# Kernel optimization log

Hardware: AMD Instinct MI355X
Metric: run time of the kernel (lower is better)

Reference implementation:

```python
import jax, jax.numpy as jnp
import numpy as np

THRESH = 0.5
ALPHA = 1.0
LOG_CLAMP = -100.0  # torch BCELoss clamps log terms at -100


def setup_inputs() -> dict:
    key = jax.random.key(0)
    k1, k2 = jax.random.split(key)
    B, N, C = 2048, 2704, 5
    # predictions: confidences/boxes in (0,1) (post-sigmoid style)
    x = jax.random.uniform(k1, (B, N, C), dtype=jnp.float32, minval=1e-3, maxval=1.0 - 1e-3)
    # labels: conf in [0,1] (~half > 0.5 -> faces), boxes in [0,1]
    y = jax.random.uniform(k2, (B, N, C), dtype=jnp.float32)
    return {"x": x, "y": y}


def _clog(v):
    return jnp.maximum(jnp.log(v), LOG_CLAMP)


def reference(x, y):
    # x, y: [B, N, 5]; channel 0 = confidence, 1:5 = box
    mask = y[..., 0] > THRESH                      # [B, N] face cells
    face_num = jnp.sum(mask).astype(x.dtype)
    bg_num = mask.size - face_num
    scale = 1.0 + 1.0 / face_num

    # MSE over masked boxes, mean over (face_num * 4) elements
    sq = jnp.sum((x[..., 1:5] - y[..., 1:5]) ** 2, axis=-1)   # [B, N]
    diff_box = scale * jnp.sum(jnp.where(mask, sq, 0.0)) / (face_num * 4.0)

    # BCE(pred_conf, label_conf) over face cells, mean
    p = x[..., 0]
    t = y[..., 0]
    bce = -(t * _clog(p) + (1.0 - t) * _clog(1.0 - p))        # [B, N]
    diff_c = scale * jnp.sum(jnp.where(mask, bce, 0.0)) / face_num

    # BCE(pred_conf, 0) over background cells, mean
    bg_bce = -_clog(1.0 - p)                                  # [B, N]
    diff_bg = ALPHA * jnp.sum(jnp.where(mask, 0.0, bg_bce)) / bg_num

    return diff_box + diff_c + diff_bg
```

## Files before the change

kernel.cpp:

```cpp
#include <hip/hip_runtime.h>


#define BLOCK 256
#define CPT 4
#define FPT (CPT * 5)
#define F4PT (FPT / 4)
#define F4_PER_BLOCK (BLOCK * F4PT)
#define PAD_STRIDE (FPT + 1)
#define LDS_FLOATS (BLOCK * PAD_STRIDE)

#define LOG_CLAMP -100.0f
#define THRESH 0.5f

__device__ __forceinline__ float clogf(float v) {
    return fmaxf(logf(v), LOG_CLAMP);
}

__global__ __launch_bounds__(BLOCK) void mloss_reduce(
    const float* __restrict__ x, const float* __restrict__ y,
    float4* __restrict__ partials)
{
    __shared__ float lx[LDS_FLOATS];
    __shared__ float ly[LDS_FLOATS];

    const long long base_f4 = (long long)blockIdx.x * F4_PER_BLOCK;
    const float4* gx = (const float4*)x + base_f4;
    const float4* gy = (const float4*)y + base_f4;

    float4 vx[F4PT], vy[F4PT];
    #pragma unroll
    for (int k = 0; k < F4PT; ++k) {
        const int i4 = threadIdx.x + k * BLOCK;
        vx[k] = gx[i4];
        vy[k] = gy[i4];
    }
    #pragma unroll
    for (int k = 0; k < F4PT; ++k) {
        const int i4 = threadIdx.x + k * BLOCK;
        const int p = 4 * i4 + i4 / 5;
        lx[p + 0] = vx[k].x; lx[p + 1] = vx[k].y; lx[p + 2] = vx[k].z; lx[p + 3] = vx[k].w;
        ly[p + 0] = vy[k].x; ly[p + 1] = vy[k].y; ly[p + 2] = vy[k].z; ly[p + 3] = vy[k].w;
    }
    __syncthreads();

    const float* mx = &lx[threadIdx.x * PAD_STRIDE];
    const float* my = &ly[threadIdx.x * PAD_STRIDE];

    float s_sq = 0.0f, s_bce = 0.0f, s_bg = 0.0f;
    float s_cnt = 0.0f;

    #pragma unroll
    for (int c = 0; c < CPT; ++c) {
        const int b = c * 5;
        const float p = mx[b];
        const float t = my[b];
        float sq = 0.0f;
        #pragma unroll
        for (int j = 1; j < 5; ++j) {
            const float d = mx[b + j] - my[b + j];
            sq = fmaf(d, d, sq);
        }
        const float lp  = clogf(p);
        const float l1p = clogf(1.0f - p);
        const bool mask = t > THRESH;
        const float bce = -(t * lp + (1.0f - t) * l1p);
        s_sq  += mask ? sq : 0.0f;
        s_bce += mask ? bce : 0.0f;
        s_bg  += mask ? 0.0f : -l1p;
        s_cnt += mask ? 1.0f : 0.0f;
    }

    #pragma unroll
    for (int off = 32; off > 0; off >>= 1) {
        s_sq  += __shfl_down(s_sq,  off, 64);
        s_bce += __shfl_down(s_bce, off, 64);
        s_bg  += __shfl_down(s_bg,  off, 64);
        s_cnt += __shfl_down(s_cnt, off, 64);
    }

    __shared__ float4 r_part[BLOCK / 64];
    const int wave = threadIdx.x >> 6;
    const int lane = threadIdx.x & 63;
    if (lane == 0) r_part[wave] = make_float4(s_sq, s_bce, s_bg, s_cnt);
    __syncthreads();
    if (threadIdx.x == 0) {
        float4 t0 = r_part[0];
        #pragma unroll
        for (int w = 1; w < BLOCK / 64; ++w) {
            t0.x += r_part[w].x; t0.y += r_part[w].y;
            t0.z += r_part[w].z; t0.w += r_part[w].w;
        }
        partials[blockIdx.x] = t0;
    }
}

#define FBLOCK 1024
__global__ __launch_bounds__(FBLOCK) void mloss_final(
    const float4* __restrict__ partials, int n_blocks,
    const float* __restrict__ x, const float* __restrict__ y,
    float* __restrict__ out, long long cell_start, long long n_cells)
{
    double s_sq = 0.0, s_bce = 0.0, s_bg = 0.0, s_cnt = 0.0;
    for (int i = threadIdx.x; i < n_blocks; i += FBLOCK) {
        const float4 v = partials[i];
        s_sq += (double)v.x; s_bce += (double)v.y;
        s_bg += (double)v.z; s_cnt += (double)v.w;
    }

    #pragma unroll
    for (int off = 32; off > 0; off >>= 1) {
        s_sq  += __shfl_down(s_sq,  off, 64);
        s_bce += __shfl_down(s_bce, off, 64);
        s_bg  += __shfl_down(s_bg,  off, 64);
        s_cnt += __shfl_down(s_cnt, off, 64);
    }

    __shared__ double r[FBLOCK / 64][4];
    const int wave = threadIdx.x >> 6;
    const int lane = threadIdx.x & 63;
    if (lane == 0) { r[wave][0] = s_sq; r[wave][1] = s_bce; r[wave][2] = s_bg; r[wave][3] = s_cnt; }
    __syncthreads();

    if (threadIdx.x == 0) {
        double t_sq = 0.0, t_bce = 0.0, t_bg = 0.0, face = 0.0;
        #pragma unroll
        for (int w = 0; w < FBLOCK / 64; ++w) {
            t_sq += r[w][0]; t_bce += r[w][1]; t_bg += r[w][2]; face += r[w][3];
        }
        for (long long c = cell_start; c < n_cells; ++c) {
            const float p = x[c * 5];
            const float t = y[c * 5];
            float sq = 0.0f;
            for (int j = 1; j < 5; ++j) {
                const float d = x[c * 5 + j] - y[c * 5 + j];
                sq = fmaf(d, d, sq);
            }
            const float lp  = clogf(p);
            const float l1p = clogf(1.0f - p);
            if (t > THRESH) {
                t_sq += (double)sq;
                t_bce += (double)(-(t * lp + (1.0f - t) * l1p));
                face += 1.0;
            } else {
                t_bg += (double)(-l1p);
            }
        }
        const double bg    = (double)n_cells - face;
        const double scale = 1.0 + 1.0 / face;
        *out = (float)(scale * t_sq / (face * 4.0) + scale * t_bce / face + t_bg / bg);
    }
}

extern "C" void kernel_launch(void* const* d_in, const int* in_sizes, int n_in,
                              void* d_out, int out_size, void* d_ws, size_t ws_size,
                              hipStream_t stream) {
    const float* x = (const float*)d_in[0];
    const float* y = (const float*)d_in[1];
    float* out = (float*)d_out;
    float4* partials = (float4*)d_ws;

    const long long n_elems = (long long)in_sizes[0];
    const long long n_cells = n_elems / 5;
    const long long cells_per_block = (long long)BLOCK * CPT;
    const long long full_blocks = n_cells / cells_per_block;
    const long long covered = full_blocks * cells_per_block;

    mloss_reduce<<<(int)full_blocks, BLOCK, 0, stream>>>(x, y, partials);
    mloss_final<<<1, FBLOCK, 0, stream>>>(partials, (int)full_blocks,
                                          x, y, out, covered, n_cells);
}
```

Before: 233.3 us.

## Replace LDS transpose with per-float4 cell-aware processing directly from global memory

Drops the shared-memory staging and transpose of 5-float cells. Each thread now loads one float4 of x and y directly and works out which lanes belong to a confidence slot and which are box terms. It re-reads the owning cell's label confidence from global memory to build the mask. This removes LDS traffic and the barrier, at the cost of an extra scattered load per float4 and more select logic per element.

```diff
diff --git a/kernel.cpp b/kernel.cpp
--- a/kernel.cpp
+++ b/kernel.cpp
@@ -2,15 +2,8 @@
 
 
 #define BLOCK 256
-#define CPT 4
-#define FPT (CPT * 5)
-#define F4PT (FPT / 4)
-#define F4_PER_BLOCK (BLOCK * F4PT)
-#define PAD_STRIDE (FPT + 1)
-#define LDS_FLOATS (BLOCK * PAD_STRIDE)
-
+#define IPT 4
 #define LOG_CLAMP -100.0f
-#define THRESH 0.5f
 
 __device__ __forceinline__ float clogf(float v) {
     return fmaxf(logf(v), LOG_CLAMP);
@@ -18,56 +11,47 @@
 
 __global__ __launch_bounds__(BLOCK) void mloss_reduce(
     const float* __restrict__ x, const float* __restrict__ y,
-    float4* __restrict__ partials)
+    float4* __restrict__ partials, long long n_groups)
 {
-    __shared__ float lx[LDS_FLOATS];
-    __shared__ float ly[LDS_FLOATS];
+    const long long base = (long long)blockIdx.x * (BLOCK * IPT) + threadIdx.x;
 
-    const long long base_f4 = (long long)blockIdx.x * F4_PER_BLOCK;
-    const float4* gx = (const float4*)x + base_f4;
-    const float4* gy = (const float4*)y + base_f4;
-
-    float4 vx[F4PT], vy[F4PT];
-    #pragma unroll
-    for (int k = 0; k < F4PT; ++k) {
-        const int i4 = threadIdx.x + k * BLOCK;
-        vx[k] = gx[i4];
-        vy[k] = gy[i4];
-    }
-    #pragma unroll
-    for (int k = 0; k < F4PT; ++k) {
-        const int i4 = threadIdx.x + k * BLOCK;
-        const int p = 4 * i4 + i4 / 5;
-        lx[p + 0] = vx[k].x; lx[p + 1] = vx[k].y; lx[p + 2] = vx[k].z; lx[p + 3] = vx[k].w;
-        ly[p + 0] = vy[k].x; ly[p + 1] = vy[k].y; ly[p + 2] = vy[k].z; ly[p + 3] = vy[k].w;
-    }
-    __syncthreads();
-
-    const float* mx = &lx[threadIdx.x * PAD_STRIDE];
-    const float* my = &ly[threadIdx.x * PAD_STRIDE];
-
-    float s_sq = 0.0f, s_bce = 0.0f, s_bg = 0.0f;
-    float s_cnt = 0.0f;
+    float s_sq = 0.0f, s_bce = 0.0f, s_bg = 0.0f, s_cnt = 0.0f;
 
     #pragma unroll
-    for (int c = 0; c < CPT; ++c) {
-        const int b = c * 5;
-        const float p = mx[b];
-        const float t = my[b];
-        float sq = 0.0f;
-        #pragma unroll
-        for (int j = 1; j < 5; ++j) {
-            const float d = mx[b + j] - my[b + j];
-            sq = fmaf(d, d, sq);
-        }
-        const float lp  = clogf(p);
-        const float l1p = clogf(1.0f - p);
-        const bool mask = t > THRESH;
-        const float bce = -(t * lp + (1.0f - t) * l1p);
-        s_sq  += mask ? sq : 0.0f;
-        s_bce += mask ? bce : 0.0f;
-        s_bg  += mask ? 0.0f : -l1p;
-        s_cnt += mask ? 1.0f : 0.0f;
+    for (int k = 0; k < IPT; ++k) {
+        const long long g = base + (long long)k * BLOCK;
+        if (g >= n_groups) break;
+        const long long e0 = g * 4;
+        const int r = (int)(e0 % 5);
+
+        const float4 x4 = ((const float4*)x)[g];
+        const float4 y4 = ((const float4*)y)[g];
+        const float  yc = y[e0 - r];
+
+        const int jc = (5 - r) % 5;
+        const float tnext = (jc == 0) ? y4.x : (jc == 1) ? y4.y : (jc == 2) ? y4.z : y4.w;
+        const float pconf = (jc == 0) ? x4.x : (jc == 1) ? x4.y : (jc == 2) ? x4.z : x4.w;
+        const bool  has_conf = (r != 1);
+
+        const float lp  = clogf(pconf);
+        const float l1p = clogf(1.0f - pconf);
+        const bool  mc  = tnext > 0.5f;
+        s_bce += (has_conf && mc)  ? -(tnext * lp + (1.0f - tnext) * l1p) : 0.0f;
+        s_bg  += (has_conf && !mc) ? -l1p : 0.0f;
+        s_cnt += (has_conf && mc)  ? 1.0f : 0.0f;
+
+        #define MLOSS_BOX(J, XJ, YJ) do {                                     \
+            const int   m  = r + (J);                                         \
+            const bool  ic = (m == 0) || (m == 5);                            \
+            const float tj = (m >= 5) ? tnext : yc;                           \
+            const float d  = (XJ) - (YJ);                                     \
+            s_sq += (!ic && tj > 0.5f) ? d * d : 0.0f;                        \
+        } while (0)
+        MLOSS_BOX(0, x4.x, y4.x);
+        MLOSS_BOX(1, x4.y, y4.y);
+        MLOSS_BOX(2, x4.z, y4.z);
+        MLOSS_BOX(3, x4.w, y4.w);
+        #undef MLOSS_BOX
     }
 
     #pragma unroll
@@ -96,12 +80,13 @@
 
 #define FBLOCK 1024
 __global__ __launch_bounds__(FBLOCK) void mloss_final(
-    const float4* __restrict__ partials, int n_blocks,
+    const float4* __restrict__ partials, int n_parts,
     const float* __restrict__ x, const float* __restrict__ y,
-    float* __restrict__ out, long long cell_start, long long n_cells)
+    float* __restrict__ out, long long elem_start, long long n_elems,
+    long long n_cells)
 {
     double s_sq = 0.0, s_bce = 0.0, s_bg = 0.0, s_cnt = 0.0;
-    for (int i = threadIdx.x; i < n_blocks; i += FBLOCK) {
+    for (int i = threadIdx.x; i < n_parts; i += FBLOCK) {
         const float4 v = partials[i];
         s_sq += (double)v.x; s_bce += (double)v.y;
         s_bg += (double)v.z; s_cnt += (double)v.w;
@@ -127,22 +112,20 @@
         for (int w = 0; w < FBLOCK / 64; ++w) {
             t_sq += r[w][0]; t_bce += r[w][1]; t_bg += r[w][2]; face += r[w][3];
         }
-        for (long long c = cell_start; c < n_cells; ++c) {
-            const float p = x[c * 5];
-            const float t = y[c * 5];
-            float sq = 0.0f;
-            for (int j = 1; j < 5; ++j) {
-                const float d = x[c * 5 + j] - y[c * 5 + j];
-                sq = fmaf(d, d, sq);
-            }
-            const float lp  = clogf(p);
-            const float l1p = clogf(1.0f - p);
-            if (t > THRESH) {
-                t_sq += (double)sq;
-                t_bce += (double)(-(t * lp + (1.0f - t) * l1p));
-                face += 1.0;
-            } else {
-                t_bg += (double)(-l1p);
+        for (long long e = elem_start; e < n_elems; ++e) {
+            const long long m  = e % 5;
+            const long long cb = e - m;
+            const float t_cell = y[cb];
+            const bool  mask   = t_cell > 0.5f;
+            if (m == 0) {
+                const float p   = x[e];
+                const float lp  = clogf(p);
+                const float l1p = clogf(1.0f - p);
+                if (mask) { t_bce += (double)(-(t_cell * lp + (1.0f - t_cell) * l1p)); face += 1.0; }
+                else      { t_bg  += (double)(-l1p); }
+            } else if (mask) {
+                const float d = x[e] - y[e];
+                t_sq += (double)(d * d);
             }
         }
         const double bg    = (double)n_cells - face;
@@ -159,13 +142,15 @@
     float* out = (float*)d_out;
     float4* partials = (float4*)d_ws;
 
-    const long long n_elems = (long long)in_sizes[0];
-    const long long n_cells = n_elems / 5;
-    const long long cells_per_block = (long long)BLOCK * CPT;
-    const long long full_blocks = n_cells / cells_per_block;
-    const long long covered = full_blocks * cells_per_block;
+    const long long n_elems  = (long long)in_sizes[0];
+    const long long n_cells  = n_elems / 5;
+    const long long n_groups = n_elems / 4;
+    const long long covered  = n_groups * 4;
 
-    mloss_reduce<<<(int)full_blocks, BLOCK, 0, stream>>>(x, y, partials);
-    mloss_final<<<1, FBLOCK, 0, stream>>>(partials, (int)full_blocks,
-                                          x, y, out, covered, n_cells);
+    const long long gpb    = (long long)BLOCK * IPT;
+    const int       blocks = (int)((n_groups + gpb - 1) / gpb);
+
+    mloss_reduce<<<blocks, BLOCK, 0, stream>>>(x, y, partials, n_groups);
+    mloss_final<<<1, FBLOCK, 0, stream>>>(partials, blocks, x, y, out,
+                                          covered, n_elems, n_cells);
 }
```

After: 237.2 us. Within noise of the previous version (+1.7%).
